# Optimization experiments

Hardware: AMD Instinct MI355X
Metric: run time of the kernel (lower is better)

Reference implementation:

```python
import jax, jax.numpy as jnp
import numpy as np

B, N, D_IN, D_MEM, LAYERS = 8, 2048, 128, 128, 3


def setup_inputs() -> dict:
    key = jax.random.key(0)
    k1, k2, k3, k4 = jax.random.split(key, 4)
    inputs = jax.random.normal(k1, (B, N, D_IN), dtype=jnp.float32)
    # attention-derived adjacency: nonnegative weights
    out_adj = jax.random.uniform(k2, (B, N, N), dtype=jnp.float32)
    # per-layer Linear weights (all layers 128->128 here, stacked) with
    # torch nn.Linear-style init scale 1/sqrt(fan_in)
    scale = 1.0 / np.sqrt(D_IN)
    W = jax.random.uniform(k3, (LAYERS, D_IN, D_MEM), minval=-scale, maxval=scale, dtype=jnp.float32)
    b = jax.random.uniform(k4, (LAYERS, D_MEM), minval=-scale, maxval=scale, dtype=jnp.float32)
    return {"inputs": inputs, "out_adj": out_adj, "W": W, "b": b}


def reference(inputs, out_adj, W, b):
    # GCN.forward (eval mode; dropout = identity)
    adj = out_adj  # [B, N, N]
    denom = jnp.sum(adj, axis=2, keepdims=True) + 1.0  # [B, N, 1]
    outputs = inputs  # [B, N, D]
    for l in range(W.shape[0]):
        Ax = jnp.einsum('bij,bjd->bid', adj, outputs)      # aggregate
        AxW = Ax @ W[l] + b[l]                             # per-layer linear
        outputs = jax.nn.relu(AxW / denom)                 # normalize + activate
    return outputs
```

## Files before the change

### kernel.cpp

```cpp
#include <hip/hip_runtime.h>

#define NN 2048
#define DD 128

typedef _Float16 f16x8 __attribute__((ext_vector_type(8)));
typedef float f32x4 __attribute__((ext_vector_type(4)));


__global__ __launch_bounds__(256) void prepAll_kernel(
    const float* __restrict__ adj, _Float16* __restrict__ adjH,
    float* __restrict__ rdg, const float* __restrict__ X,
    _Float16* __restrict__ Xt, const float* __restrict__ W,
    _Float16* __restrict__ Wt) {
  __shared__ float rs[16][4];
  const int bx = blockIdx.x, tid = threadIdx.x;
  const int lane = tid & 63, wave = tid >> 6;
  const int quad = lane >> 4, l15 = lane & 15;

  if (bx < 1024) {
    const int it = bx & 127, batch = bx >> 7;
    const float* Ap = adj + ((size_t)(batch * NN) + it * 16 + l15) * NN + quad * 8;
    _Float16* Hp = adjH + (size_t)batch * NN * NN + ((size_t)it * 64) * 512 + lane * 8;
    float s = 0.f;
#pragma unroll
    for (int j = 0; j < 16; ++j) {
      const int ct = wave + 4 * j;
      float4 a0 = *(const float4*)(Ap + ct * 32);
      float4 a1 = *(const float4*)(Ap + ct * 32 + 4);
      s += ((a0.x + a0.y) + (a0.z + a0.w)) + ((a1.x + a1.y) + (a1.z + a1.w));
      f16x8 h = {(_Float16)a0.x, (_Float16)a0.y, (_Float16)a0.z, (_Float16)a0.w,
                 (_Float16)a1.x, (_Float16)a1.y, (_Float16)a1.z, (_Float16)a1.w};
      *(f16x8*)(Hp + (size_t)ct * 512) = h;
    }
    s += __shfl_xor(s, 16);
    s += __shfl_xor(s, 32);
    if (lane < 16) rs[lane][wave] = s;
    __syncthreads();
    if (tid < 16) {
      float t = rs[tid][0] + rs[tid][1] + rs[tid][2] + rs[tid][3];
      rdg[batch * NN + it * 16 + tid] = 1.0f / (t + 1.0f);
    }
  } else if (bx < 1536) {
    const int vbx = bx - 1024;
    const int batch = vbx & 7, nt = vbx >> 3;
    const size_t batA = (size_t)batch * (128 * NN);
#pragma unroll
    for (int dtl = 0; dtl < 2; ++dtl) {
      const int dt = wave * 2 + dtl;
      const float* Xp = X + ((size_t)(batch * NN) + nt * 32 + quad * 8) * DD + dt * 16 + l15;
      f16x8 v;
#pragma unroll
      for (int e = 0; e < 8; ++e) v[e] = (_Float16)Xp[(size_t)e * DD];
      *(f16x8*)(Xt + batA + ((size_t)(dt * 64 + nt)) * 512 + lane * 8) = v;
    }
  } else {
    int idx = (bx - 1536) * 256 + tid;
    int l = idx >> 14, r = idx & 16383, d = r >> 7, k = r & 127;
    Wt[idx] = (_Float16)W[l * 16384 + k * 128 + d];
  }
}

__device__ __forceinline__ void epiGemm(const float (*Xs)[132],
    const _Float16* __restrict__ Wf, int d0, int quad, int l15,
    f32x4 (&o)[2][2]) {
#pragma unroll
  for (int kk = 0; kk < 128; kk += 32) {
    f16x8 a0 = *(const f16x8*)(Wf + (d0 + l15) * DD + kk + quad * 8);
    f16x8 a1 = *(const f16x8*)(Wf + (d0 + 16 + l15) * DD + kk + quad * 8);
#pragma unroll
    for (int fi = 0; fi < 2; ++fi) {
      const float* xp = &Xs[fi * 16 + l15][kk + quad * 8];
      f16x8 b = {(_Float16)xp[0], (_Float16)xp[1], (_Float16)xp[2], (_Float16)xp[3],
                 (_Float16)xp[4], (_Float16)xp[5], (_Float16)xp[6], (_Float16)xp[7]};
      o[0][fi] = __builtin_amdgcn_mfma_f32_16x16x32_f16(a0, b, o[0][fi], 0, 0, 0);
      o[1][fi] = __builtin_amdgcn_mfma_f32_16x16x32_f16(a1, b, o[1][fi], 0, 0, 0);
    }
  }
}

__device__ __forceinline__ void aggMainC(const _Float16* __restrict__ At,
    const _Float16* __restrict__ adjHb, size_t batA, size_t batB,
    int wave, int lane, int iblk, _Float16* __restrict__ Bs,
    f32x4 (&acc)[2][2]) {
  const int it0 = iblk * 2;
  const _Float16* Ap0 = At + batA + ((size_t)(2 * wave) * 64) * 512 + lane * 8;
  const _Float16* Ap1 = At + batA + ((size_t)(2 * wave + 1) * 64) * 512 + lane * 8;
  const _Float16* Bq0 = adjHb + batB + ((size_t)it0 * 64) * 512 + lane * 8;
  const _Float16* Bq1 = adjHb + batB + ((size_t)(it0 + 1) * 64) * 512 + lane * 8;

  const int t0 = wave * 4;

  f16x8 sreg[4];
#pragma unroll
  for (int j = 0; j < 4; ++j) {
    const int t = t0 + j, cl = t >> 1, rt = t & 1;
    sreg[j] = *(const f16x8*)((rt ? Bq1 : Bq0) + (size_t)cl * 512);
  }
  f16x8 qa0[4], qa1[4];
#pragma unroll
  for (int j = 0; j < 4; ++j) {
    qa0[j] = *(const f16x8*)(Ap0 + (size_t)j * 512);
    qa1[j] = *(const f16x8*)(Ap1 + (size_t)j * 512);
  }

#pragma unroll
  for (int ch = 0; ch < 8; ++ch) {
    _Float16* buf = Bs + (ch & 1) * (16 * 512);
#pragma unroll
    for (int j = 0; j < 4; ++j)
      *(f16x8*)(buf + (t0 + j) * 512 + lane * 8) = sreg[j];
    if (ch < 7) {
#pragma unroll
      for (int j = 0; j < 4; ++j) {
        const int t = t0 + j, cl = t >> 1, rt = t & 1;
        sreg[j] = *(const f16x8*)((rt ? Bq1 : Bq0) +
                                  (size_t)((ch + 1) * 8 + cl) * 512);
      }
    }
    __syncthreads();
#pragma unroll
    for (int c = 0; c < 8; ++c) {
      const int ct = ch * 8 + c;
      const int s = ct & 3;
      f16x8 b0 = *(const f16x8*)(buf + (c * 2 + 0) * 512 + lane * 8);
      f16x8 b1 = *(const f16x8*)(buf + (c * 2 + 1) * 512 + lane * 8);
      acc[0][0] = __builtin_amdgcn_mfma_f32_16x16x32_f16(qa0[s], b0, acc[0][0], 0, 0, 0);
      acc[0][1] = __builtin_amdgcn_mfma_f32_16x16x32_f16(qa0[s], b1, acc[0][1], 0, 0, 0);
      acc[1][0] = __builtin_amdgcn_mfma_f32_16x16x32_f16(qa1[s], b0, acc[1][0], 0, 0, 0);
      acc[1][1] = __builtin_amdgcn_mfma_f32_16x16x32_f16(qa1[s], b1, acc[1][1], 0, 0, 0);
      if (ct + 4 < 64) {
        qa0[s] = *(const f16x8*)(Ap0 + (size_t)(ct + 4) * 512);
        qa1[s] = *(const f16x8*)(Ap1 + (size_t)(ct + 4) * 512);
      }
    }
  }
}

__device__ __forceinline__ void fragStoreY(float (*Xs)[132],
    const f32x4 (&accY)[2][2], _Float16* __restrict__ Yb, int i0,
    int wave, int quad, int l15, int lane, int d0) {
  __syncthreads();
  _Float16* Yst = (_Float16*)Xs;
#pragma unroll
  for (int df = 0; df < 2; ++df)
#pragma unroll
    for (int fi = 0; fi < 2; ++fi)
#pragma unroll
      for (int r = 0; r < 4; ++r)
        Yst[(d0 + df * 16 + quad * 4 + r) * 40 + fi * 16 + l15] =
            (_Float16)accY[df][fi][r];
  __syncthreads();
  const int nt = i0 >> 5;
#pragma unroll
  for (int dtl = 0; dtl < 2; ++dtl) {
    const int dt = 2 * wave + dtl;
    f16x8 v = *(const f16x8*)(&Yst[(dt * 16 + l15) * 40 + quad * 8]);
    *(f16x8*)(Yb + ((size_t)(dt * 64 + nt)) * 512 + lane * 8) = v;
  }
}

template<int MODE>
__global__ __launch_bounds__(256, 4) void aggC_kernel(
    const _Float16* __restrict__ adjH, const float* __restrict__ rdg,
    const _Float16* __restrict__ At, const float* __restrict__ bias,
    const _Float16* __restrict__ WA, const _Float16* __restrict__ WB,
    _Float16* __restrict__ Yout, float* __restrict__ out) {
  __shared__ __align__(16) char smem[2 * 16 * 512 * sizeof(_Float16)];
  __shared__ float bsh[128];
  __shared__ float rdsh[32];
  _Float16* Bs = (_Float16*)smem;
  float (*Xs)[132] = (float(*)[132])smem;

  const int tid = threadIdx.x, bx = blockIdx.x;
  const int batch = bx & 7, iblk = bx >> 3, i0 = iblk * 32;
  const int lane = tid & 63, wave = tid >> 6;
  const int quad = lane >> 4, l15 = lane & 15, d0 = wave * 32;

  const size_t batA = (size_t)batch * (128 * NN);
  const size_t batB = (size_t)batch * ((size_t)NN * NN);

  if (tid < 128) bsh[tid] = bias[tid];
  if (tid < 32) rdsh[tid] = rdg[batch * NN + i0 + tid];

  f32x4 acc[2][2] = {};
  aggMainC(At, adjH, batA, batB, wave, lane, iblk, Bs, acc);

  __syncthreads();
  const float rv0 = rdsh[l15], rv1 = rdsh[16 + l15];
  f32x4 accY[2][2];

  if (MODE == 0) {
#pragma unroll
    for (int df = 0; df < 2; ++df)
#pragma unroll
      for (int fi = 0; fi < 2; ++fi)
#pragma unroll
        for (int r = 0; r < 4; ++r)
          Xs[fi * 16 + l15][d0 + df * 16 + quad * 4 + r] = acc[df][fi][r];
    __syncthreads();
    f32x4 acc2[2][2] = {};
    epiGemm(Xs, WA, d0, quad, l15, acc2);
    __syncthreads();
#pragma unroll
    for (int df = 0; df < 2; ++df)
#pragma unroll
      for (int fi = 0; fi < 2; ++fi)
#pragma unroll
        for (int r = 0; r < 4; ++r) {
          int d = d0 + df * 16 + quad * 4 + r;
          float rv = fi ? rv1 : rv0;
          Xs[fi * 16 + l15][d] = fmaxf((acc2[df][fi][r] + bsh[d]) * rv, 0.f);
        }
    __syncthreads();
    f32x4 acc3[2][2] = {};
    epiGemm(Xs, WB, d0, quad, l15, acc3);
#pragma unroll
    for (int df = 0; df < 2; ++df)
#pragma unroll
      for (int fi = 0; fi < 2; ++fi) accY[df][fi] = acc3[df][fi];
  } else {
#pragma unroll
    for (int df = 0; df < 2; ++df)
#pragma unroll
      for (int fi = 0; fi < 2; ++fi)
#pragma unroll
        for (int r = 0; r < 4; ++r) {
          int d = d0 + df * 16 + quad * 4 + r;
          float rv = fi ? rv1 : rv0;
          Xs[fi * 16 + l15][d] = fmaxf((acc[df][fi][r] + bsh[d]) * rv, 0.f);
        }
    __syncthreads();
    if (MODE == 2) {
      float* outB = out + (size_t)(batch * NN + i0) * DD;
#pragma unroll
      for (int u = 0; u < 4; ++u) {
        int c = tid + 256 * u;
        int i = c >> 5, f4 = (c & 31) * 4;
        *(float4*)(outB + (size_t)i * DD + f4) = *(const float4*)&Xs[i][f4];
      }
      return;
    }
    f32x4 acc2[2][2] = {};
    epiGemm(Xs, WA, d0, quad, l15, acc2);
#pragma unroll
    for (int df = 0; df < 2; ++df)
#pragma unroll
      for (int fi = 0; fi < 2; ++fi) accY[df][fi] = acc2[df][fi];
  }

  fragStoreY(Xs, accY, Yout + batA, i0, wave, quad, l15, lane, d0);
}

__global__ __launch_bounds__(256) void prep_kernel(
    const float* __restrict__ W, _Float16* __restrict__ Wt) {
  int idx = blockIdx.x * 256 + threadIdx.x;
  int l = idx >> 14, r = idx & 16383, d = r >> 7, k = r & 127;
  Wt[idx] = (_Float16)W[l * 16384 + k * 128 + d];
}

__global__ __launch_bounds__(256) void gemmY_kernel(
    const float* __restrict__ X, const _Float16* __restrict__ Wt,
    _Float16* __restrict__ Yt) {
  const int bx = blockIdx.x;
  const int batch = bx & 7, n0 = (bx >> 3) * 32;
  const int tid = threadIdx.x, lane = tid & 63, wave = tid >> 6;
  const int quad = lane >> 4, l15 = lane & 15, d0 = wave * 32;
  const float* Xb = X + (size_t)(batch * NN + n0) * DD;
  f32x4 acc[2][2] = {};
#pragma unroll
  for (int kk = 0; kk < 128; kk += 32) {
    f16x8 a0 = *(const f16x8*)(Wt + (d0 + l15) * DD + kk + quad * 8);
    f16x8 a1 = *(const f16x8*)(Wt + (d0 + 16 + l15) * DD + kk + quad * 8);
#pragma unroll
    for (int fi = 0; fi < 2; ++fi) {
      const float* xp = Xb + (size_t)(fi * 16 + l15) * DD + kk + quad * 8;
      float4 x0 = *(const float4*)xp;
      float4 x1 = *(const float4*)(xp + 4);
      f16x8 b = {(_Float16)x0.x, (_Float16)x0.y, (_Float16)x0.z, (_Float16)x0.w,
                 (_Float16)x1.x, (_Float16)x1.y, (_Float16)x1.z, (_Float16)x1.w};
      acc[0][fi] = __builtin_amdgcn_mfma_f32_16x16x32_f16(a0, b, acc[0][fi], 0, 0, 0);
      acc[1][fi] = __builtin_amdgcn_mfma_f32_16x16x32_f16(a1, b, acc[1][fi], 0, 0, 0);
    }
  }
  _Float16* YtB = Yt + (size_t)batch * DD * NN;
#pragma unroll
  for (int df = 0; df < 2; ++df)
#pragma unroll
    for (int fi = 0; fi < 2; ++fi)
#pragma unroll
      for (int r = 0; r < 4; ++r)
        YtB[(size_t)(d0 + df * 16 + quad * 4 + r) * NN + n0 + fi * 16 + l15] =
            (_Float16)acc[df][fi][r];
}

template<bool LAST>
__global__ __launch_bounds__(256) void agg_kernel(
    const float* __restrict__ adj, const _Float16* __restrict__ Yt,
    const float* __restrict__ bias, const _Float16* __restrict__ Wn,
    _Float16* __restrict__ Ytn, float* __restrict__ out) {
  __shared__ _Float16 Bsl[2][32 * 64];
  __shared__ float Xs[32][132];
  __shared__ float bsh[128];
  __shared__ float rd[32];

  const int tid = threadIdx.x, bx = blockIdx.x;
  const int batch = bx & 7, i0 = (bx >> 3) * 32;
  const int lane = tid & 63, wave = tid >> 6;
  const int quad = lane >> 4, l15 = lane & 15, d0 = wave * 32;
  const int ai = tid >> 3, ac = tid & 7;
  const int sc = ac ^ (ai & 7);

  const float* adjR = adj + (size_t)(batch * NN + i0 + ai) * NN + ac * 8;
  const _Float16* YtB = Yt + (size_t)batch * DD * NN;
  const _Float16* Ya0 = YtB + (size_t)(d0 + l15) * NN;
  const _Float16* Ya1 = YtB + (size_t)(d0 + 16 + l15) * NN;

  if (tid < 128) bsh[tid] = bias[tid];

  f32x4 acc[2][2] = {};
  float rowsum = 0.f;

  float4 av0 = *(const float4*)(adjR);
  float4 av1 = *(const float4*)(adjR + 4);
  f16x8 a[2][2];
#pragma unroll
  for (int k2 = 0; k2 < 2; ++k2) {
    a[k2][0] = *(const f16x8*)(Ya0 + k2 * 32 + quad * 8);
    a[k2][1] = *(const f16x8*)(Ya1 + k2 * 32 + quad * 8);
  }

  for (int ko = 0; ko < 32; ++ko) {
    rowsum += ((av0.x + av0.y) + (av0.z + av0.w)) + ((av1.x + av1.y) + (av1.z + av1.w));
    f16x8 h = {(_Float16)av0.x, (_Float16)av0.y, (_Float16)av0.z, (_Float16)av0.w,
               (_Float16)av1.x, (_Float16)av1.y, (_Float16)av1.z, (_Float16)av1.w};
    *(f16x8*)(&Bsl[ko & 1][ai * 64 + sc * 8]) = h;
    f16x8 an[2][2];
    if (ko < 31) {
      const int kb = (ko + 1) * 64;
      av0 = *(const float4*)(adjR + kb);
      av1 = *(const float4*)(adjR + kb + 4);
#pragma unroll
      for (int k2 = 0; k2 < 2; ++k2) {
        an[k2][0] = *(const f16x8*)(Ya0 + kb + k2 * 32 + quad * 8);
        an[k2][1] = *(const f16x8*)(Ya1 + kb + k2 * 32 + quad * 8);
      }
    }
    __syncthreads();
    const _Float16* B = Bsl[ko & 1];
#pragma unroll
    for (int k2 = 0; k2 < 2; ++k2)
#pragma unroll
      for (int fi = 0; fi < 2; ++fi) {
        const int row = fi * 16 + l15;
        const int ch = (k2 * 4 + quad) ^ (row & 7);
        f16x8 b = *(const f16x8*)(&B[row * 64 + ch * 8]);
        acc[0][fi] = __builtin_amdgcn_mfma_f32_16x16x32_f16(a[k2][0], b, acc[0][fi], 0, 0, 0);
        acc[1][fi] = __builtin_amdgcn_mfma_f32_16x16x32_f16(a[k2][1], b, acc[1][fi], 0, 0, 0);
      }
#pragma unroll
    for (int k2 = 0; k2 < 2; ++k2) { a[k2][0] = an[k2][0]; a[k2][1] = an[k2][1]; }
  }

  rowsum += __shfl_xor(rowsum, 1);
  rowsum += __shfl_xor(rowsum, 2);
  rowsum += __shfl_xor(rowsum, 4);
  if (ac == 0) rd[ai] = 1.0f / (rowsum + 1.0f);
  __syncthreads();

#pragma unroll
  for (int df = 0; df < 2; ++df)
#pragma unroll
    for (int fi = 0; fi < 2; ++fi)
#pragma unroll
      for (int r = 0; r < 4; ++r) {
        int d = d0 + df * 16 + quad * 4 + r;
        int i = fi * 16 + l15;
        Xs[i][d] = fmaxf((acc[df][fi][r] + bsh[d]) * rd[i], 0.f);
      }
  __syncthreads();

  if (LAST) {
    float* outB = out + (size_t)(batch * NN + i0) * DD;
#pragma unroll
    for (int u = 0; u < 4; ++u) {
      int c = tid + 256 * u;
      int i = c >> 5, f4 = (c & 31) * 4;
      *(float4*)(outB + (size_t)i * DD + f4) = *(const float4*)&Xs[i][f4];
    }
  } else {
    f32x4 acc2[2][2] = {};
    epiGemm(Xs, Wn, d0, quad, l15, acc2);
    _Float16* YnB = Ytn + (size_t)batch * DD * NN;
#pragma unroll
    for (int df = 0; df < 2; ++df)
#pragma unroll
      for (int fi = 0; fi < 2; ++fi)
#pragma unroll
        for (int r = 0; r < 4; ++r)
          YnB[(size_t)(d0 + df * 16 + quad * 4 + r) * NN + i0 + fi * 16 + l15] =
              (_Float16)acc2[df][fi][r];
  }
}

extern "C" void kernel_launch(void* const* d_in, const int* in_sizes, int n_in,
                              void* d_out, int out_size, void* d_ws, size_t ws_size,
                              hipStream_t stream) {
  const float* x0   = (const float*)d_in[0];
  const float* adj  = (const float*)d_in[1];
  const float* W    = (const float*)d_in[2];
  const float* bias = (const float*)d_in[3];
  float* out = (float*)d_out;

  _Float16* Wt   = (_Float16*)d_ws;
  float*    rdg  = (float*)((char*)d_ws + (1u << 17));
  _Float16* Xt   = (_Float16*)((char*)d_ws + (1u << 20));
  _Float16* Y1t  = (_Float16*)((char*)d_ws + (5u << 20));
  _Float16* Y2t  = (_Float16*)((char*)d_ws + (9u << 20));
  _Float16* adjH = (_Float16*)((char*)d_ws + (16u << 20));

  const bool big = ws_size >= (81ull << 20);
  dim3 blk(256);

  if (big) {
    prepAll_kernel<<<1728, blk, 0, stream>>>(adj, adjH, rdg, x0, Xt, W, Wt);
    aggC_kernel<0><<<512, blk, 0, stream>>>(adjH, rdg, Xt, bias, Wt, Wt + 16384, Y1t, nullptr);
    aggC_kernel<1><<<512, blk, 0, stream>>>(adjH, rdg, Y1t, bias + 128, Wt + 32768, nullptr, Y2t, nullptr);
    aggC_kernel<2><<<512, blk, 0, stream>>>(adjH, rdg, Y2t, bias + 256, nullptr, nullptr, nullptr, out);
  } else {
    _Float16* YtA  = Xt;
    _Float16* YtB_ = (_Float16*)d_out;
    prep_kernel<<<192, blk, 0, stream>>>(W, Wt);
    gemmY_kernel<<<512, blk, 0, stream>>>(x0, Wt, YtA);
    agg_kernel<false><<<512, blk, 0, stream>>>(adj, YtA,  bias,       Wt + 16384, YtB_, nullptr);
    agg_kernel<false><<<512, blk, 0, stream>>>(adj, YtB_, bias + 128, Wt + 32768, YtA,  nullptr);
    agg_kernel<true ><<<512, blk, 0, stream>>>(adj, YtA,  bias + 256, nullptr,    nullptr, out);
  }
}
```

Measured before the change: 271.8 us.

## Fuse adjacency fp16 conversion and row sums into first aggregation kernel

The fp32 adjacency conversion to fp16 and the row-sum normalisation move out of the prep kernel and into a new first-layer aggregation kernel. That kernel reads fp32 adj directly, converts each chunk into shared memory for the MFMA aggregation, and writes the fp16 copy and reciprocal degrees for later layers. This removes a separate pass that read all of adj and then re-read its fp16 copy, so the first layer consumes adj in the same pass that converts it. In exchange the fused kernel issues more global loads per block, carries extra register pressure for the prefetched fp32 tiles, and may be less bandwidth-efficient than the standalone conversion.

```diff
diff --git a/kernel.cpp b/kernel.cpp
--- a/kernel.cpp
+++ b/kernel.cpp
@@ -7,42 +7,14 @@
 typedef float f32x4 __attribute__((ext_vector_type(4)));
 
 
-__global__ __launch_bounds__(256) void prepAll_kernel(
-    const float* __restrict__ adj, _Float16* __restrict__ adjH,
-    float* __restrict__ rdg, const float* __restrict__ X,
-    _Float16* __restrict__ Xt, const float* __restrict__ W,
-    _Float16* __restrict__ Wt) {
-  __shared__ float rs[16][4];
+__global__ __launch_bounds__(256) void prepX_kernel(
+    const float* __restrict__ X, _Float16* __restrict__ Xt,
+    const float* __restrict__ W, _Float16* __restrict__ Wt) {
   const int bx = blockIdx.x, tid = threadIdx.x;
   const int lane = tid & 63, wave = tid >> 6;
   const int quad = lane >> 4, l15 = lane & 15;
-
-  if (bx < 1024) {
-    const int it = bx & 127, batch = bx >> 7;
-    const float* Ap = adj + ((size_t)(batch * NN) + it * 16 + l15) * NN + quad * 8;
-    _Float16* Hp = adjH + (size_t)batch * NN * NN + ((size_t)it * 64) * 512 + lane * 8;
-    float s = 0.f;
-#pragma unroll
-    for (int j = 0; j < 16; ++j) {
-      const int ct = wave + 4 * j;
-      float4 a0 = *(const float4*)(Ap + ct * 32);
-      float4 a1 = *(const float4*)(Ap + ct * 32 + 4);
-      s += ((a0.x + a0.y) + (a0.z + a0.w)) + ((a1.x + a1.y) + (a1.z + a1.w));
-      f16x8 h = {(_Float16)a0.x, (_Float16)a0.y, (_Float16)a0.z, (_Float16)a0.w,
-                 (_Float16)a1.x, (_Float16)a1.y, (_Float16)a1.z, (_Float16)a1.w};
-      *(f16x8*)(Hp + (size_t)ct * 512) = h;
-    }
-    s += __shfl_xor(s, 16);
-    s += __shfl_xor(s, 32);
-    if (lane < 16) rs[lane][wave] = s;
-    __syncthreads();
-    if (tid < 16) {
-      float t = rs[tid][0] + rs[tid][1] + rs[tid][2] + rs[tid][3];
-      rdg[batch * NN + it * 16 + tid] = 1.0f / (t + 1.0f);
-    }
-  } else if (bx < 1536) {
-    const int vbx = bx - 1024;
-    const int batch = vbx & 7, nt = vbx >> 3;
+  if (bx < 512) {
+    const int batch = bx & 7, nt = bx >> 3;
     const size_t batA = (size_t)batch * (128 * NN);
 #pragma unroll
     for (int dtl = 0; dtl < 2; ++dtl) {
@@ -54,7 +26,7 @@
       *(f16x8*)(Xt + batA + ((size_t)(dt * 64 + nt)) * 512 + lane * 8) = v;
     }
   } else {
-    int idx = (bx - 1536) * 256 + tid;
+    int idx = (bx - 512) * 256 + tid;
     int l = idx >> 14, r = idx & 16383, d = r >> 7, k = r & 127;
     Wt[idx] = (_Float16)W[l * 16384 + k * 128 + d];
   }
@@ -159,12 +131,140 @@
   }
 }
 
+__global__ __launch_bounds__(256, 4) void aggF_kernel(
+    const float* __restrict__ adj, _Float16* __restrict__ adjH,
+    float* __restrict__ rdg, const _Float16* __restrict__ Xt,
+    const float* __restrict__ bias, const _Float16* __restrict__ W0f,
+    const _Float16* __restrict__ W1f, _Float16* __restrict__ Y1t) {
+  __shared__ __align__(16) char smem[2 * 16 * 512 * sizeof(_Float16)];
+  __shared__ float bsh[128];
+  __shared__ float rdsh[32];
+  __shared__ float rs2[2][16][4];
+  _Float16* Bs = (_Float16*)smem;
+  float (*Xs)[132] = (float(*)[132])smem;
+
+  const int tid = threadIdx.x, bx = blockIdx.x;
+  const int batch = bx & 7, iblk = bx >> 3, i0 = iblk * 32;
+  const int lane = tid & 63, wave = tid >> 6;
+  const int quad = lane >> 4, l15 = lane & 15, d0 = wave * 32;
+  const size_t batA = (size_t)batch * (128 * NN);
+  const size_t batB = (size_t)batch * ((size_t)NN * NN);
+  const int it0 = iblk * 2;
+
+  if (tid < 128) bsh[tid] = bias[tid];
+
+  const _Float16* Ap0 = Xt + batA + ((size_t)(2 * wave) * 64) * 512 + lane * 8;
+  const _Float16* Ap1 = Xt + batA + ((size_t)(2 * wave + 1) * 64) * 512 + lane * 8;
+
+  const float* AdjB = adj + ((size_t)(batch * NN + i0)) * NN;
+  const float* rp[4];
+#pragma unroll
+  for (int j = 0; j < 4; ++j)
+    rp[j] = AdjB + (size_t)((j & 1) * 16 + l15) * NN + (2 * wave + (j >> 1)) * 32 + quad * 8;
+
+  const int t0 = wave * 4;
+  float rsum0 = 0.f, rsum1 = 0.f;
+  float4 sa[4], sb[4];
+  f16x8 qa0[4], qa1[4];
+
+#pragma unroll
+  for (int j = 0; j < 4; ++j) { sa[j] = *(const float4*)(rp[j]); sb[j] = *(const float4*)(rp[j] + 4); }
+#pragma unroll
+  for (int j = 0; j < 4; ++j) {
+    qa0[j] = *(const f16x8*)(Ap0 + (size_t)j * 512);
+    qa1[j] = *(const f16x8*)(Ap1 + (size_t)j * 512);
+  }
+
+  f32x4 acc[2][2] = {};
+
+#pragma unroll
+  for (int ch = 0; ch < 8; ++ch) {
+    _Float16* buf = Bs + (ch & 1) * (16 * 512);
+#pragma unroll
+    for (int j = 0; j < 4; ++j) {
+      float4 a0 = sa[j], a1 = sb[j];
+      float s = ((a0.x + a0.y) + (a0.z + a0.w)) + ((a1.x + a1.y) + (a1.z + a1.w));
+      if (j & 1) rsum1 += s; else rsum0 += s;
+      f16x8 h = {(_Float16)a0.x, (_Float16)a0.y, (_Float16)a0.z, (_Float16)a0.w,
+                 (_Float16)a1.x, (_Float16)a1.y, (_Float16)a1.z, (_Float16)a1.w};
+      *(f16x8*)(buf + (t0 + j) * 512 + lane * 8) = h;
+      *(f16x8*)(adjH + batB +
+                ((size_t)((it0 + (j & 1)) * 64 + ch * 8 + 2 * wave + (j >> 1))) * 512 +
+                lane * 8) = h;
+    }
+    if (ch < 7) {
+#pragma unroll
+      for (int j = 0; j < 4; ++j) {
+        sa[j] = *(const float4*)(rp[j] + (ch + 1) * 256);
+        sb[j] = *(const float4*)(rp[j] + (ch + 1) * 256 + 4);
+      }
+    }
+    __syncthreads();
+#pragma unroll
+    for (int c = 0; c < 8; ++c) {
+      const int ct = ch * 8 + c;
+      const int s = ct & 3;
+      f16x8 b0 = *(const f16x8*)(buf + (c * 2 + 0) * 512 + lane * 8);
+      f16x8 b1 = *(const f16x8*)(buf + (c * 2 + 1) * 512 + lane * 8);
+      acc[0][0] = __builtin_amdgcn_mfma_f32_16x16x32_f16(qa0[s], b0, acc[0][0], 0, 0, 0);
+      acc[0][1] = __builtin_amdgcn_mfma_f32_16x16x32_f16(qa0[s], b1, acc[0][1], 0, 0, 0);
+      acc[1][0] = __builtin_amdgcn_mfma_f32_16x16x32_f16(qa1[s], b0, acc[1][0], 0, 0, 0);
+      acc[1][1] = __builtin_amdgcn_mfma_f32_16x16x32_f16(qa1[s], b1, acc[1][1], 0, 0, 0);
+      if (ct + 4 < 64) {
+        qa0[s] = *(const f16x8*)(Ap0 + (size_t)(ct + 4) * 512);
+        qa1[s] = *(const f16x8*)(Ap1 + (size_t)(ct + 4) * 512);
+      }
+    }
+  }
+
+  rsum0 += __shfl_xor(rsum0, 16);
+  rsum0 += __shfl_xor(rsum0, 32);
+  rsum1 += __shfl_xor(rsum1, 16);
+  rsum1 += __shfl_xor(rsum1, 32);
+  if (lane < 16) { rs2[0][lane][wave] = rsum0; rs2[1][lane][wave] = rsum1; }
+  __syncthreads();
+  if (tid < 32) {
+    const int rt = tid >> 4, r = tid & 15;
+    float t = rs2[rt][r][0] + rs2[rt][r][1] + rs2[rt][r][2] + rs2[rt][r][3];
+    float v = 1.0f / (t + 1.0f);
+    rdsh[tid] = v;
+    rdg[batch * NN + i0 + tid] = v;
+  }
+
+#pragma unroll
+  for (int df = 0; df < 2; ++df)
+#pragma unroll
+    for (int fi = 0; fi < 2; ++fi)
+#pragma unroll
+      for (int r = 0; r < 4; ++r)
+        Xs[fi * 16 + l15][d0 + df * 16 + quad * 4 + r] = acc[df][fi][r];
+  __syncthreads();
+  f32x4 acc2[2][2] = {};
+  epiGemm(Xs, W0f, d0, quad, l15, acc2);
+  __syncthreads();
+  const float rv0 = rdsh[l15], rv1 = rdsh[16 + l15];
+#pragma unroll
+  for (int df = 0; df < 2; ++df)
+#pragma unroll
+    for (int fi = 0; fi < 2; ++fi)
+#pragma unroll
+      for (int r = 0; r < 4; ++r) {
+        int d = d0 + df * 16 + quad * 4 + r;
+        float rv = fi ? rv1 : rv0;
+        Xs[fi * 16 + l15][d] = fmaxf((acc2[df][fi][r] + bsh[d]) * rv, 0.f);
+      }
+  __syncthreads();
+  f32x4 acc3[2][2] = {};
+  epiGemm(Xs, W1f, d0, quad, l15, acc3);
+  fragStoreY(Xs, acc3, Y1t + batA, i0, wave, quad, l15, lane, d0);
+}
+
 template<int MODE>
 __global__ __launch_bounds__(256, 4) void aggC_kernel(
     const _Float16* __restrict__ adjH, const float* __restrict__ rdg,
     const _Float16* __restrict__ At, const float* __restrict__ bias,
-    const _Float16* __restrict__ WA, const _Float16* __restrict__ WB,
-    _Float16* __restrict__ Yout, float* __restrict__ out) {
+    const _Float16* __restrict__ WA, _Float16* __restrict__ Yout,
+    float* __restrict__ out) {
   __shared__ __align__(16) char smem[2 * 16 * 512 * sizeof(_Float16)];
   __shared__ float bsh[128];
   __shared__ float rdsh[32];
@@ -187,68 +287,31 @@
 
   __syncthreads();
   const float rv0 = rdsh[l15], rv1 = rdsh[16 + l15];
-  f32x4 accY[2][2];
-
-  if (MODE == 0) {
-#pragma unroll
-    for (int df = 0; df < 2; ++df)
-#pragma unroll
-      for (int fi = 0; fi < 2; ++fi)
-#pragma unroll
-        for (int r = 0; r < 4; ++r)
-          Xs[fi * 16 + l15][d0 + df * 16 + quad * 4 + r] = acc[df][fi][r];
-    __syncthreads();
-    f32x4 acc2[2][2] = {};
-    epiGemm(Xs, WA, d0, quad, l15, acc2);
-    __syncthreads();
-#pragma unroll
-    for (int df = 0; df < 2; ++df)
-#pragma unroll
-      for (int fi = 0; fi < 2; ++fi)
-#pragma unroll
-        for (int r = 0; r < 4; ++r) {
-          int d = d0 + df * 16 + quad * 4 + r;
-          float rv = fi ? rv1 : rv0;
-          Xs[fi * 16 + l15][d] = fmaxf((acc2[df][fi][r] + bsh[d]) * rv, 0.f);
-        }
-    __syncthreads();
-    f32x4 acc3[2][2] = {};
-    epiGemm(Xs, WB, d0, quad, l15, acc3);
-#pragma unroll
-    for (int df = 0; df < 2; ++df)
-#pragma unroll
-      for (int fi = 0; fi < 2; ++fi) accY[df][fi] = acc3[df][fi];
-  } else {
-#pragma unroll
-    for (int df = 0; df < 2; ++df)
-#pragma unroll
-      for (int fi = 0; fi < 2; ++fi)
-#pragma unroll
-        for (int r = 0; r < 4; ++r) {
-          int d = d0 + df * 16 + quad * 4 + r;
-          float rv = fi ? rv1 : rv0;
-          Xs[fi * 16 + l15][d] = fmaxf((acc[df][fi][r] + bsh[d]) * rv, 0.f);
-        }
-    __syncthreads();
-    if (MODE == 2) {
-      float* outB = out + (size_t)(batch * NN + i0) * DD;
-#pragma unroll
-      for (int u = 0; u < 4; ++u) {
-        int c = tid + 256 * u;
-        int i = c >> 5, f4 = (c & 31) * 4;
-        *(float4*)(outB + (size_t)i * DD + f4) = *(const float4*)&Xs[i][f4];
-      }
-      return;
-    }
-    f32x4 acc2[2][2] = {};
-    epiGemm(Xs, WA, d0, quad, l15, acc2);
-#pragma unroll
-    for (int df = 0; df < 2; ++df)
-#pragma unroll
-      for (int fi = 0; fi < 2; ++fi) accY[df][fi] = acc2[df][fi];
-  }
-
-  fragStoreY(Xs, accY, Yout + batA, i0, wave, quad, l15, lane, d0);
+
+#pragma unroll
+  for (int df = 0; df < 2; ++df)
+#pragma unroll
+    for (int fi = 0; fi < 2; ++fi)
+#pragma unroll
+      for (int r = 0; r < 4; ++r) {
+        int d = d0 + df * 16 + quad * 4 + r;
+        float rv = fi ? rv1 : rv0;
+        Xs[fi * 16 + l15][d] = fmaxf((acc[df][fi][r] + bsh[d]) * rv, 0.f);
+      }
+  __syncthreads();
+  if (MODE == 2) {
+    float* outB = out + (size_t)(batch * NN + i0) * DD;
+#pragma unroll
+    for (int u = 0; u < 4; ++u) {
+      int c = tid + 256 * u;
+      int i = c >> 5, f4 = (c & 31) * 4;
+      *(float4*)(outB + (size_t)i * DD + f4) = *(const float4*)&Xs[i][f4];
+    }
+    return;
+  }
+  f32x4 acc2[2][2] = {};
+  epiGemm(Xs, WA, d0, quad, l15, acc2);
+  fragStoreY(Xs, acc2, Yout + batA, i0, wave, quad, l15, lane, d0);
 }
 
 __global__ __launch_bounds__(256) void prep_kernel(
@@ -422,10 +485,10 @@
   dim3 blk(256);
 
   if (big) {
-    prepAll_kernel<<<1728, blk, 0, stream>>>(adj, adjH, rdg, x0, Xt, W, Wt);
-    aggC_kernel<0><<<512, blk, 0, stream>>>(adjH, rdg, Xt, bias, Wt, Wt + 16384, Y1t, nullptr);
-    aggC_kernel<1><<<512, blk, 0, stream>>>(adjH, rdg, Y1t, bias + 128, Wt + 32768, nullptr, Y2t, nullptr);
-    aggC_kernel<2><<<512, blk, 0, stream>>>(adjH, rdg, Y2t, bias + 256, nullptr, nullptr, nullptr, out);
+    prepX_kernel<<<704, blk, 0, stream>>>(x0, Xt, W, Wt);
+    aggF_kernel<<<512, blk, 0, stream>>>(adj, adjH, rdg, Xt, bias, Wt, Wt + 16384, Y1t);
+    aggC_kernel<1><<<512, blk, 0, stream>>>(adjH, rdg, Y1t, bias + 128, Wt + 32768, Y2t, nullptr);
+    aggC_kernel<2><<<512, blk, 0, stream>>>(adjH, rdg, Y2t, bias + 256, nullptr, nullptr, out);
   } else {
     _Float16* YtA  = Xt;
     _Float16* YtB_ = (_Float16*)d_out;
```

Measured after the change: 267.6 us. No clear change (-1.5%).
